# Performance work log

Hardware: AMD Instinct MI355X
Metric: run time of the kernel (lower is better)

The kernel has to match this reference:

```python
import jax, jax.numpy as jnp
import numpy as np

VOCAB = 10000
HID = 256
BATCH = 32
STEPS = 256


def setup_inputs() -> dict:
    key = jax.random.key(0)
    ks = jax.random.split(key, 8)
    X = jax.random.randint(ks[0], (BATCH, STEPS), 0, VOCAB)
    H = jnp.zeros((BATCH, HID), dtype=jnp.float32)
    s = 0.01
    inp = {
        "X": X,
        "H": H,
        "W_xz": jax.random.normal(ks[1], (VOCAB, HID), jnp.float32) * s,
        "W_hz": jax.random.normal(ks[2], (HID, HID), jnp.float32) * s,
        "b_z": jnp.zeros((HID,), jnp.float32),
        "W_xr": jax.random.normal(ks[3], (VOCAB, HID), jnp.float32) * s,
        "W_hr": jax.random.normal(ks[4], (HID, HID), jnp.float32) * s,
        "b_r": jnp.zeros((HID,), jnp.float32),
        "W_xh": jax.random.normal(ks[5], (VOCAB, HID), jnp.float32) * s,
        "W_hh": jax.random.normal(ks[6], (HID, HID), jnp.float32) * s,
        "b_h": jnp.zeros((HID,), jnp.float32),
        "W_hq": jax.random.normal(ks[7], (HID, VOCAB), jnp.float32) * s,
        "b_q": jnp.zeros((VOCAB,), jnp.float32),
    }
    return inp


def reference(X, H, W_xz, W_hz, b_z, W_xr, W_hr, b_r, W_xh, W_hh, b_h, W_hq, b_q):
    # one-hot of X.T -> (steps, batch, vocab) float32
    Xo = jax.nn.one_hot(X.T, VOCAB, dtype=jnp.float32)

    def step(h, x):  # x: (batch, vocab), h: (batch, hid)
        z = jax.nn.sigmoid(x @ W_xz + h @ W_hz + b_z)
        r = jax.nn.sigmoid(x @ W_xr + h @ W_hr + b_r)
        h_tilda = jnp.tanh(x @ W_xh + (r * h) @ W_hh + b_h)
        h_new = z * h + (1.0 - z) * h_tilda
        y = h_new @ W_hq + b_q  # (batch, vocab)
        return h_new, y

    H_final, Ys = jax.lax.scan(step, H, Xo)
    out = Ys.reshape(STEPS * BATCH, VOCAB)  # matches torch.cat(outputs, dim=0)
    return out, (H_final,)
```

## Files before the change

kernel.cpp:

```cpp
#include <hip/hip_runtime.h>
#include <hip/hip_bf16.h>
#include <stdint.h>

#define VOCAB 10000
#define HID   256
#define BATCH 32
#define STEPS 256

typedef __attribute__((ext_vector_type(8))) short short8;
typedef __attribute__((ext_vector_type(4))) float floatx4;

__device__ __forceinline__ float bf2f(unsigned short u) {
    union { unsigned int ui; float f; } v;
    v.ui = ((unsigned int)u) << 16;
    return v.f;
}

__device__ __forceinline__ unsigned short f2bf(float f) {
    union { float f; unsigned int ui; } v;
    v.f = f;
    unsigned int u = v.ui;
    unsigned int r = (u + 0x7FFFu + ((u >> 16) & 1u)) >> 16;
    return (unsigned short)r;
}

#if __has_builtin(__builtin_amdgcn_fdot2_f32_bf16)
typedef __bf16 bf16x2 __attribute__((ext_vector_type(2)));
__device__ __forceinline__ float dot2(unsigned int w, unsigned int h, float acc) {
    union { unsigned int u; bf16x2 v; } a, b;
    a.u = w; b.u = h;
    return __builtin_amdgcn_fdot2_f32_bf16(a.v, b.v, acc, false);
}
#else
__device__ __forceinline__ float dot2(unsigned int w, unsigned int h, float acc) {
    union { unsigned int u; float f; } w0, w1, h0, h1;
    w0.u = w << 16; w1.u = w & 0xFFFF0000u;
    h0.u = h << 16; h1.u = h & 0xFFFF0000u;
    acc = fmaf(w0.f, h0.f, acc);
    acc = fmaf(w1.f, h1.f, acc);
    return acc;
}
#endif

__device__ __forceinline__ float sigmoidf_(float x) {
    return __builtin_amdgcn_rcpf(1.0f + __expf(-x));
}
__device__ __forceinline__ float tanhf_(float x) {
    float e = __expf(2.0f * x);
    return 1.0f - 2.0f * __builtin_amdgcn_rcpf(e + 1.0f);
}

__global__ void prep_w(const float* __restrict__ Wz, const float* __restrict__ Wr,
                       const float* __restrict__ Wh, unsigned short* __restrict__ out) {
    int g = blockIdx.x, p4 = blockIdx.y, j = threadIdx.x;
    const float* W = (g == 0) ? Wz : (g == 1) ? Wr : Wh;
    union { unsigned short us[8]; short8 v; } pk;
    #pragma unroll
    for (int m = 0; m < 8; ++m)
        pk.us[m] = f2bf(W[(p4 * 8 + m) * HID + j]);
    *(short8*)(out + (((size_t)g * 32 + p4) * HID + j) * 8) = pk.v;
}

__global__ void prep_b(const float* __restrict__ Whq, unsigned short* __restrict__ bfr) {
    __shared__ float lds[32][257];
    const int nb = blockIdx.x;
    const int kc = blockIdx.y;
    const int tid = threadIdx.x;
    const int n0 = nb * 256;

    #pragma unroll 4
    for (int kk = 0; kk < 32; ++kk) {
        int n = n0 + tid;
        float v = (n < VOCAB) ? Whq[(size_t)(kc * 32 + kk) * VOCAB + n] : 0.0f;
        lds[kk][tid] = v;
    }
    __syncthreads();

    const int lane = tid & 63;
    const int wq   = tid >> 6;
    const int quad = lane >> 4, l15 = lane & 15;
    #pragma unroll
    for (int ntp = 0; ntp < 4; ++ntp) {
        int nt_local = ntp * 4 + wq;
        int nt = nb * 16 + nt_local;
        if (nt >= 625) continue;
        union { unsigned short us[8]; short8 v; } pk;
        #pragma unroll
        for (int jj = 0; jj < 8; ++jj)
            pk.us[jj] = f2bf(lds[quad * 8 + jj][nt_local * 16 + l15]);
        *(short8*)(bfr + (((size_t)nt * 8 + kc) * 64 + lane) * 8) = pk.v;
    }
}

__global__ __launch_bounds__(256) void prep_a(const unsigned short* __restrict__ hist,
                                              unsigned short* __restrict__ afr) {
    __shared__ __align__(16) unsigned short tile[16 * 256];
    const int MT = blockIdx.x;
    const int tid = threadIdx.x;

    const uint4* src = (const uint4*)(hist + (size_t)MT * 16 * 256);
    uint4* dst = (uint4*)tile;
    dst[tid]       = src[tid];
    dst[tid + 256] = src[tid + 256];
    __syncthreads();

    #pragma unroll
    for (int i = 0; i < 2; ++i) {
        int s = tid * 2 + i;
        int kc = s >> 6, lane = s & 63;
        int quad = lane >> 4, l15 = lane & 15;
        const unsigned short* p = tile + l15 * 256 + kc * 32 + quad * 8;
        *(short8*)(afr + (((size_t)MT * 8 + kc) * 64 + lane) * 8) = *(const short8*)p;
    }
}

__global__ __launch_bounds__(512, 1) void gru_rec(
    const int* __restrict__ X, const float* __restrict__ H0,
    const float* __restrict__ Wxz, const float* __restrict__ Wxr,
    const float* __restrict__ Wxh,
    const float* __restrict__ bz, const float* __restrict__ br,
    const float* __restrict__ bh,
    const unsigned short* __restrict__ Wsw,
    unsigned short* __restrict__ hist,
    float* __restrict__ h_final)
{
    const int b = blockIdx.x;
    const int tid = threadIdx.x;
    const bool isA = tid < HID;
    const int j = isA ? tid : tid - HID;

    __shared__ __align__(16) unsigned short hbuf[HID];
    __shared__ __align__(16) unsigned short rhbuf[HID];
    __shared__ float part[HID];
    __shared__ float xrow[2][3][HID];
    __shared__ int Xl[STEPS];

    const uint4* wA = (const uint4*)Wsw + (size_t)(isA ? 0 : 1) * 32 * HID + j;
    const uint4* wH = (const uint4*)Wsw + (size_t)2 * 32 * HID + j;

    float h_my = H0[b * HID + j];
    float bias = isA ? bz[j] : br[j];
    float bhj  = isA ? bh[j] : 0.0f;

    uint4 wreg[32];
    #pragma unroll
    for (int i = 0; i < 32; ++i) wreg[i] = wA[i * HID];

    const int i0 = isA ? 0 : 16;
    uint4 whreg[16];
    #pragma unroll
    for (int i = 0; i < 16; ++i) whreg[i] = wH[(i0 + i) * HID];

    if (isA) { hbuf[j] = f2bf(h_my); Xl[j] = X[b * STEPS + j]; }
    __syncthreads();

    {
        int x0 = Xl[0];
        if (isA) {
            xrow[0][0][j] = Wxz[(size_t)x0 * HID + j];
            xrow[0][2][j] = Wxh[(size_t)x0 * HID + j];
        } else {
            xrow[0][1][j] = Wxr[(size_t)x0 * HID + j];
        }
    }
    __syncthreads();

    float z = 0.0f;

    for (int t = 0; t < STEPS; ++t) {
        const int cur = t & 1, nxt = cur ^ 1;

        const int xn = Xl[(t + 1) & (STEPS - 1)];
        float p0 = 0.f, p1 = 0.f;
        if (isA) {
            p0 = Wxz[(size_t)xn * HID + j];
            p1 = Wxh[(size_t)xn * HID + j];
        } else {
            p0 = Wxr[(size_t)xn * HID + j];
        }

        float acc;
        {
            const uint4* hp = (const uint4*)hbuf;
            float a0 = 0.f, a1 = 0.f, a2 = 0.f, a3 = 0.f;
            #pragma unroll
            for (int i = 0; i < 32; ++i) {
                uint4 hv = hp[i];
                a0 = dot2(wreg[i].x, hv.x, a0);
                a1 = dot2(wreg[i].y, hv.y, a1);
                a2 = dot2(wreg[i].z, hv.z, a2);
                a3 = dot2(wreg[i].w, hv.w, a3);
            }
            acc = (a0 + a1) + (a2 + a3);
        }

        if (isA) {
            z = sigmoidf_(acc + xrow[cur][0][j] + bias);
            xrow[nxt][0][j] = p0;
            xrow[nxt][2][j] = p1;
        } else {
            float r = sigmoidf_(acc + xrow[cur][1][j] + bias);
            rhbuf[j] = f2bf(r * h_my);
            xrow[nxt][1][j] = p0;
        }
        __syncthreads();

        float acch;
        {
            const uint4* rp = (const uint4*)rhbuf;
            float a0 = 0.f, a1 = 0.f, a2 = 0.f, a3 = 0.f;
            #pragma unroll
            for (int i = 0; i < 16; ++i) {
                uint4 hv = rp[i0 + i];
                a0 = dot2(whreg[i].x, hv.x, a0);
                a1 = dot2(whreg[i].y, hv.y, a1);
                a2 = dot2(whreg[i].z, hv.z, a2);
                a3 = dot2(whreg[i].w, hv.w, a3);
            }
            acch = (a0 + a1) + (a2 + a3);
        }
        if (!isA) part[j] = acch;
        __syncthreads();

        if (isA) {
            float hpre = acch + part[j] + xrow[cur][2][j] + bhj;
            float ht = tanhf_(hpre);
            float hn = z * h_my + (1.0f - z) * ht;
            h_my = hn;
            unsigned short hb = f2bf(hn);
            hbuf[j] = hb;
            hist[((size_t)t * BATCH + b) * HID + j] = hb;
        }
        __syncthreads();

        if (!isA) h_my = bf2f(hbuf[j]);
    }

    if (isA) h_final[b * HID + j] = h_my;
}

__global__ __launch_bounds__(256, 2) void proj(
    const unsigned short* __restrict__ Afr,
    const unsigned short* __restrict__ Bfr,
    const float* __restrict__ bq,
    float* __restrict__ C)
{
    const int tid  = threadIdx.x;
    const int wave = tid >> 6;
    const int lane = tid & 63;
    const int l15  = lane & 15;
    const int quad = lane >> 4;

    const int orig = blockIdx.x;
    const int xcd  = orig & 7;
    const int idx  = orig >> 3;
    const int mb   = idx / 5;
    const int nb   = xcd * 5 + (idx % 5);

    const int m0 = mb * 128;
    const int nt0 = nb * 16 + wave * 4;

    floatx4 acc[8][4];
    #pragma unroll
    for (int i = 0; i < 8; ++i)
        #pragma unroll
        for (int q = 0; q < 4; ++q)
            acc[i][q] = (floatx4)0.0f;

    int ntc[4];
    #pragma unroll
    for (int q = 0; q < 4; ++q) {
        int nt = nt0 + q;
        ntc[q] = (nt < 625) ? nt : 624;
    }

    for (int kc = 0; kc < 8; ++kc) {
        short8 a[8];
        #pragma unroll
        for (int mt = 0; mt < 8; ++mt) {
            const unsigned short* ap =
                Afr + (((size_t)(mb * 8 + mt) * 8 + kc) * 64 + lane) * 8;
            a[mt] = *(const short8*)ap;
        }
        short8 bfrg[4];
        #pragma unroll
        for (int q = 0; q < 4; ++q) {
            const unsigned short* bp =
                Bfr + ((((size_t)ntc[q] * 8 + kc) * 64) + lane) * 8;
            bfrg[q] = *(const short8*)bp;
        }
        #pragma unroll
        for (int mt = 0; mt < 8; ++mt)
            #pragma unroll
            for (int q = 0; q < 4; ++q)
                acc[mt][q] = __builtin_amdgcn_mfma_f32_16x16x32_bf16(
                    bfrg[q], a[mt], acc[mt][q], 0, 0, 0);
    }

    floatx4 bq4[4];
    #pragma unroll
    for (int q = 0; q < 4; ++q) {
        int nt = nt0 + q;
        bq4[q] = (nt < 625) ? *(const floatx4*)(bq + nt * 16 + quad * 4)
                            : (floatx4)0.0f;
    }
    #pragma unroll
    for (int mt = 0; mt < 8; ++mt) {
        const size_t rowoff = (size_t)(m0 + mt * 16 + l15) * VOCAB;
        #pragma unroll
        for (int q = 0; q < 4; ++q) {
            int nt = nt0 + q;
            if (nt >= 625) continue;
            floatx4 v = acc[mt][q] + bq4[q];
            __builtin_nontemporal_store(v, (floatx4*)(C + rowoff + nt * 16 + quad * 4));
        }
    }
}

extern "C" void kernel_launch(void* const* d_in, const int* in_sizes, int n_in,
                              void* d_out, int out_size, void* d_ws, size_t ws_size,
                              hipStream_t stream) {
    const int*   X   = (const int*)  d_in[0];
    const float* H0  = (const float*)d_in[1];
    const float* Wxz = (const float*)d_in[2];
    const float* Whz = (const float*)d_in[3];
    const float* bz  = (const float*)d_in[4];
    const float* Wxr = (const float*)d_in[5];
    const float* Whr = (const float*)d_in[6];
    const float* br  = (const float*)d_in[7];
    const float* Wxh = (const float*)d_in[8];
    const float* Whh = (const float*)d_in[9];
    const float* bh  = (const float*)d_in[10];
    const float* Whq = (const float*)d_in[11];
    const float* bq  = (const float*)d_in[12];

    float* out     = (float*)d_out;
    float* h_final = out + (size_t)STEPS * BATCH * VOCAB;

    unsigned short* wsw  = (unsigned short*)d_ws;
    unsigned short* bfr  = wsw + 196608;
    unsigned short* hist = bfr + 2560000;
    unsigned short* afr  = hist + 2097152;

    prep_w<<<dim3(3, 32), 256, 0, stream>>>(Whz, Whr, Whh, wsw);
    prep_b<<<dim3(40, 8), 256, 0, stream>>>(Whq, bfr);
    gru_rec<<<BATCH, 512, 0, stream>>>(X, H0, Wxz, Wxr, Wxh, bz, br, bh,
                                       wsw, hist, h_final);
    prep_a<<<512, 256, 0, stream>>>(hist, afr);
    proj<<<2560, 256, 0, stream>>>(afr, bfr, bq, out);
}
```

Baseline: 809.5 us.

## Collapse GRU recurrence to one thread per hidden unit with all gate weights

The recurrent kernel now runs 256 threads per batch row instead of 512, and each thread holds the z, r and candidate weight columns in registers. The partial-sum exchange through shared memory is gone, as are one barrier per step and the final reload of h. The cost is about 384 VGPRs of weights per thread and twice the serial dot-product work per thread each step. The higher register pressure may spill and lengthen the critical path.

```diff
diff --git a/kernel.cpp b/kernel.cpp
--- a/kernel.cpp
+++ b/kernel.cpp
@@ -114,7 +114,7 @@
     }
 }
 
-__global__ __launch_bounds__(512, 1) void gru_rec(
+__global__ __launch_bounds__(256, 1) void gru_rec(
     const int* __restrict__ X, const float* __restrict__ H0,
     const float* __restrict__ Wxz, const float* __restrict__ Wxr,
     const float* __restrict__ Wxh,
@@ -125,118 +125,97 @@
     float* __restrict__ h_final)
 {
     const int b = blockIdx.x;
-    const int tid = threadIdx.x;
-    const bool isA = tid < HID;
-    const int j = isA ? tid : tid - HID;
+    const int j = threadIdx.x;
 
     __shared__ __align__(16) unsigned short hbuf[HID];
     __shared__ __align__(16) unsigned short rhbuf[HID];
-    __shared__ float part[HID];
     __shared__ float xrow[2][3][HID];
     __shared__ int Xl[STEPS];
 
-    const uint4* wA = (const uint4*)Wsw + (size_t)(isA ? 0 : 1) * 32 * HID + j;
-    const uint4* wH = (const uint4*)Wsw + (size_t)2 * 32 * HID + j;
+    const uint4* wz = (const uint4*)Wsw + j;
+    const uint4* wr = (const uint4*)Wsw + (size_t)1 * 32 * HID + j;
+    const uint4* wh = (const uint4*)Wsw + (size_t)2 * 32 * HID + j;
 
     float h_my = H0[b * HID + j];
-    float bias = isA ? bz[j] : br[j];
-    float bhj  = isA ? bh[j] : 0.0f;
-
-    uint4 wreg[32];
-    #pragma unroll
-    for (int i = 0; i < 32; ++i) wreg[i] = wA[i * HID];
-
-    const int i0 = isA ? 0 : 16;
-    uint4 whreg[16];
-    #pragma unroll
-    for (int i = 0; i < 16; ++i) whreg[i] = wH[(i0 + i) * HID];
-
-    if (isA) { hbuf[j] = f2bf(h_my); Xl[j] = X[b * STEPS + j]; }
+    const float bzj = bz[j], brj = br[j], bhj = bh[j];
+
+    uint4 wzreg[32], wrreg[32], whreg[32];
+    #pragma unroll
+    for (int i = 0; i < 32; ++i) wzreg[i] = wz[i * HID];
+    #pragma unroll
+    for (int i = 0; i < 32; ++i) wrreg[i] = wr[i * HID];
+    #pragma unroll
+    for (int i = 0; i < 32; ++i) whreg[i] = wh[i * HID];
+
+    hbuf[j] = f2bf(h_my);
+    Xl[j] = X[b * STEPS + j];
     __syncthreads();
 
     {
         int x0 = Xl[0];
-        if (isA) {
-            xrow[0][0][j] = Wxz[(size_t)x0 * HID + j];
-            xrow[0][2][j] = Wxh[(size_t)x0 * HID + j];
-        } else {
-            xrow[0][1][j] = Wxr[(size_t)x0 * HID + j];
-        }
+        xrow[0][0][j] = Wxz[(size_t)x0 * HID + j];
+        xrow[0][1][j] = Wxr[(size_t)x0 * HID + j];
+        xrow[0][2][j] = Wxh[(size_t)x0 * HID + j];
     }
     __syncthreads();
-
-    float z = 0.0f;
 
     for (int t = 0; t < STEPS; ++t) {
         const int cur = t & 1, nxt = cur ^ 1;
 
         const int xn = Xl[(t + 1) & (STEPS - 1)];
-        float p0 = 0.f, p1 = 0.f;
-        if (isA) {
-            p0 = Wxz[(size_t)xn * HID + j];
-            p1 = Wxh[(size_t)xn * HID + j];
-        } else {
-            p0 = Wxr[(size_t)xn * HID + j];
-        }
-
-        float acc;
+        float p0 = Wxz[(size_t)xn * HID + j];
+        float p1 = Wxr[(size_t)xn * HID + j];
+        float p2 = Wxh[(size_t)xn * HID + j];
+
+        float z0 = 0.f, z1 = 0.f, z2 = 0.f, z3 = 0.f;
+        float r0 = 0.f, r1 = 0.f, r2 = 0.f, r3 = 0.f;
         {
             const uint4* hp = (const uint4*)hbuf;
-            float a0 = 0.f, a1 = 0.f, a2 = 0.f, a3 = 0.f;
             #pragma unroll
             for (int i = 0; i < 32; ++i) {
                 uint4 hv = hp[i];
-                a0 = dot2(wreg[i].x, hv.x, a0);
-                a1 = dot2(wreg[i].y, hv.y, a1);
-                a2 = dot2(wreg[i].z, hv.z, a2);
-                a3 = dot2(wreg[i].w, hv.w, a3);
+                z0 = dot2(wzreg[i].x, hv.x, z0);
+                z1 = dot2(wzreg[i].y, hv.y, z1);
+                z2 = dot2(wzreg[i].z, hv.z, z2);
+                z3 = dot2(wzreg[i].w, hv.w, z3);
+                r0 = dot2(wrreg[i].x, hv.x, r0);
+                r1 = dot2(wrreg[i].y, hv.y, r1);
+                r2 = dot2(wrreg[i].z, hv.z, r2);
+                r3 = dot2(wrreg[i].w, hv.w, r3);
             }
-            acc = (a0 + a1) + (a2 + a3);
-        }
-
-        if (isA) {
-            z = sigmoidf_(acc + xrow[cur][0][j] + bias);
-            xrow[nxt][0][j] = p0;
-            xrow[nxt][2][j] = p1;
-        } else {
-            float r = sigmoidf_(acc + xrow[cur][1][j] + bias);
-            rhbuf[j] = f2bf(r * h_my);
-            xrow[nxt][1][j] = p0;
-        }
+        }
+        float z = sigmoidf_(((z0 + z1) + (z2 + z3)) + xrow[cur][0][j] + bzj);
+        float r = sigmoidf_(((r0 + r1) + (r2 + r3)) + xrow[cur][1][j] + brj);
+        rhbuf[j] = f2bf(r * h_my);
         __syncthreads();
 
-        float acch;
+        float a0 = 0.f, a1 = 0.f, a2 = 0.f, a3 = 0.f;
         {
             const uint4* rp = (const uint4*)rhbuf;
-            float a0 = 0.f, a1 = 0.f, a2 = 0.f, a3 = 0.f;
             #pragma unroll
-            for (int i = 0; i < 16; ++i) {
-                uint4 hv = rp[i0 + i];
+            for (int i = 0; i < 32; ++i) {
+                uint4 hv = rp[i];
                 a0 = dot2(whreg[i].x, hv.x, a0);
                 a1 = dot2(whreg[i].y, hv.y, a1);
                 a2 = dot2(whreg[i].z, hv.z, a2);
                 a3 = dot2(whreg[i].w, hv.w, a3);
             }
-            acch = (a0 + a1) + (a2 + a3);
-        }
-        if (!isA) part[j] = acch;
+        }
+        float hpre = ((a0 + a1) + (a2 + a3)) + xrow[cur][2][j] + bhj;
+        float ht = tanhf_(hpre);
+        float hn = z * h_my + (1.0f - z) * ht;
+        h_my = hn;
+        unsigned short hb = f2bf(hn);
+        hist[((size_t)t * BATCH + b) * HID + j] = hb;
+
+        xrow[nxt][0][j] = p0;
+        xrow[nxt][1][j] = p1;
+        xrow[nxt][2][j] = p2;
+        hbuf[j] = hb;
         __syncthreads();
-
-        if (isA) {
-            float hpre = acch + part[j] + xrow[cur][2][j] + bhj;
-            float ht = tanhf_(hpre);
-            float hn = z * h_my + (1.0f - z) * ht;
-            h_my = hn;
-            unsigned short hb = f2bf(hn);
-            hbuf[j] = hb;
-            hist[((size_t)t * BATCH + b) * HID + j] = hb;
-        }
-        __syncthreads();
-
-        if (!isA) h_my = bf2f(hbuf[j]);
-    }
-
-    if (isA) h_final[b * HID + j] = h_my;
+    }
+
+    h_final[b * HID + j] = h_my;
 }
 
 __global__ __launch_bounds__(256, 2) void proj(
@@ -344,7 +323,7 @@
 
     prep_w<<<dim3(3, 32), 256, 0, stream>>>(Whz, Whr, Whh, wsw);
     prep_b<<<dim3(40, 8), 256, 0, stream>>>(Whq, bfr);
-    gru_rec<<<BATCH, 512, 0, stream>>>(X, H0, Wxz, Wxr, Wxh, bz, br, bh,
+    gru_rec<<<BATCH, 256, 0, stream>>>(X, H0, Wxz, Wxr, Wxh, bz, br, bh,
                                        wsw, hist, h_final);
     prep_a<<<512, 256, 0, stream>>>(hist, afr);
     proj<<<2560, 256, 0, stream>>>(afr, bfr, bq, out);
```

Result: slower. 1.181 ms (+45.9%).
